# Optimization experiments

Hardware: AMD Instinct MI355X
Metric: run time of the kernel (lower is better)

The kernel has to match this reference:

```python
import jax, jax.numpy as jnp
import numpy as np

M, K, N = 8192, 4096, 4096

def setup_inputs() -> dict:
    key = jax.random.key(0)
    k0, k1, k2, k3, k4 = jax.random.split(key, 5)
    x = jax.random.normal(k0, (M, K), dtype=jnp.float32)
    # int8 weight stored as int32 spec dtype; values in [-127, 127]
    weight = jax.random.randint(k1, (N, K), -127, 128, dtype=jnp.int32)
    input_scale = jnp.array([0.02], dtype=jnp.float32)
    input_offset = jnp.zeros((1,), dtype=jnp.int32)
    # per-output-channel dequant scale (small positive)
    deq_scale = jax.random.uniform(k2, (N,), dtype=jnp.float32, minval=1e-4, maxval=2e-4)
    quant_bias = jax.random.randint(k3, (N,), -100, 101, dtype=jnp.int32)
    # sparse-compression output-channel reorder index (a permutation)
    index = jax.random.permutation(k4, N).astype(jnp.int32)
    return {"x": x, "weight": weight, "input_scale": input_scale,
            "input_offset": input_offset, "deq_scale": deq_scale,
            "quant_bias": quant_bias, "index": index}

def reference(x, weight, input_scale, input_offset, deq_scale, quant_bias, index):
    # 1) per-tensor activation quantization to int8
    x_q = jnp.clip(jnp.round(x / input_scale) + input_offset.astype(jnp.float32),
                   -128.0, 127.0).astype(jnp.int8)
    acc = jnp.matmul(x_q.astype(jnp.int32), weight.astype(jnp.int8).astype(jnp.int32).T)
    acc = acc + quant_bias  # [M, N] int32
    # 3) per-channel dequantization
    y = acc.astype(jnp.float32) * deq_scale  # [M, N]
    # 4) restore output-channel order from compressed layout
    return jnp.take(y, index, axis=-1)
```

## Files before the change

### kernel.cpp

```cpp
#include <hip/hip_runtime.h>
#include <hip/hip_bf16.h>
#include <stdint.h>

#define M_DIM 8192
#define K_DIM 4096
#define N_DIM 4096

#define BM 128
#define BN 128
#define BK 128

typedef int i32x4 __attribute__((ext_vector_type(4)));

__global__ __launch_bounds__(256) void quant_x_kernel(
    const float* __restrict__ x, const float* __restrict__ scale_p,
    const int* __restrict__ off_p, int8_t* __restrict__ xq)
{
    const float s = scale_p[0];
    const float off = (float)off_p[0];
    long base = ((long)blockIdx.x * 256 + threadIdx.x) * 16;
    const float4* xin = (const float4*)(x + base);
    float v[16];
    *(float4*)(v + 0)  = xin[0];
    *(float4*)(v + 4)  = xin[1];
    *(float4*)(v + 8)  = xin[2];
    *(float4*)(v + 12) = xin[3];
    uint32_t pk[4];
#pragma unroll
    for (int g = 0; g < 4; ++g) {
        uint32_t p = 0;
#pragma unroll
        for (int j = 0; j < 4; ++j) {
            float q = rintf(v[g * 4 + j] / s) + off;
            q = fminf(fmaxf(q, -128.0f), 127.0f);
            int qi = (int)q;
            p |= ((uint32_t)(qi & 0xff)) << (8 * j);
        }
        pk[g] = p;
    }
    uint4 o; o.x = pk[0]; o.y = pk[1]; o.z = pk[2]; o.w = pk[3];
    *(uint4*)(xq + base) = o;
}

__global__ __launch_bounds__(256) void pack_w_kernel(
    const int* __restrict__ w, const int* __restrict__ index,
    const float* __restrict__ deq, const int* __restrict__ qb,
    int8_t* __restrict__ bp, float* __restrict__ dsp, int* __restrict__ qbp)
{
    int j = blockIdx.x;
    int t = threadIdx.x;
    int src = index[j];
    const int4* wrow = (const int4*)(w + (long)src * K_DIM);
    uint32_t pk[4];
#pragma unroll
    for (int g = 0; g < 4; ++g) {
        int4 c = wrow[t * 4 + g];
        pk[g] = ((uint32_t)(c.x & 0xff)) | (((uint32_t)(c.y & 0xff)) << 8) |
                (((uint32_t)(c.z & 0xff)) << 16) | (((uint32_t)(c.w & 0xff)) << 24);
    }
    uint4 o; o.x = pk[0]; o.y = pk[1]; o.z = pk[2]; o.w = pk[3];
    *(uint4*)(bp + (long)j * K_DIM + t * 16) = o;
    if (t == 0) { dsp[j] = deq[src]; qbp[j] = qb[src]; }
}

__device__ __forceinline__ void gload_lds16(const void* g, void* l)
{
    __builtin_amdgcn_global_load_lds(
        (const __attribute__((address_space(1))) uint32_t*)g,
        (__attribute__((address_space(3))) uint32_t*)l, 16, 0, 0);
}

__global__ __launch_bounds__(256) void gemm_i8_kernel(
    const int8_t* __restrict__ A, const int8_t* __restrict__ B,
    const float* __restrict__ dsp, const int* __restrict__ qbp,
    float* __restrict__ C)
{
    __shared__ int8_t As[BM * BK];
    __shared__ int8_t Bs[BN * BK];

    int bid = blockIdx.x;
    int cpx = gridDim.x >> 3;
    int swz = (bid & 7) * cpx + (bid >> 3);
    int bn = swz % (N_DIM / BN);
    int bm = swz / (N_DIM / BN);
    int brow = bm * BM, bcol = bn * BN;

    int t = threadIdx.x;
    int l = t & 63;
    int wv = t >> 6;
    int wr = (wv >> 1) * 64;
    int wc = (wv & 1) * 64;

    const int8_t* ga[4];
    const int8_t* gb[4];
#pragma unroll
    for (int i = 0; i < 4; ++i) {
        int cid = i * 256 + t;
        int row = cid >> 3;
        int p = cid & 7;
        int lg = p ^ (row & 7);
        ga[i] = A + (long)(brow + row) * K_DIM + lg * 16;
        gb[i] = B + (long)(bcol + row) * K_DIM + lg * 16;
    }

    i32x4 acc[4][4] = {};

    for (int kt = 0; kt < K_DIM / BK; ++kt) {
#pragma unroll
        for (int i = 0; i < 4; ++i) {
            gload_lds16(ga[i], As + (i * 256 + t) * 16);
            ga[i] += BK;
        }
#pragma unroll
        for (int i = 0; i < 4; ++i) {
            gload_lds16(gb[i], Bs + (i * 256 + t) * 16);
            gb[i] += BK;
        }
        __syncthreads();

#pragma unroll
        for (int kk = 0; kk < 2; ++kk) {
            i32x4 af[4], bf[4];
#pragma unroll
            for (int m = 0; m < 4; ++m) {
                int row = wr + m * 16 + (l & 15);
                int slot = (kk * 4 + (l >> 4)) ^ (row & 7);
                af[m] = *(const i32x4*)(As + row * BK + slot * 16);
            }
#pragma unroll
            for (int n = 0; n < 4; ++n) {
                int row = wc + n * 16 + (l & 15);
                int slot = (kk * 4 + (l >> 4)) ^ (row & 7);
                bf[n] = *(const i32x4*)(Bs + row * BK + slot * 16);
            }
#pragma unroll
            for (int m = 0; m < 4; ++m)
#pragma unroll
                for (int n = 0; n < 4; ++n)
                    acc[m][n] = __builtin_amdgcn_mfma_i32_16x16x64_i8(
                        af[m], bf[n], acc[m][n], 0, 0, 0);
        }
        __syncthreads();
    }

#pragma unroll
    for (int n = 0; n < 4; ++n) {
        int gc = bcol + wc + n * 16 + (l & 15);
        float ds = dsp[gc];
        int qb = qbp[gc];
#pragma unroll
        for (int m = 0; m < 4; ++m) {
            int gr0 = brow + wr + m * 16 + ((l >> 4) * 4);
#pragma unroll
            for (int r = 0; r < 4; ++r) {
                float val = (float)(acc[m][n][r] + qb) * ds;
                C[(long)(gr0 + r) * N_DIM + gc] = val;
            }
        }
    }
}

extern "C" void kernel_launch(void* const* d_in, const int* in_sizes, int n_in,
                              void* d_out, int out_size, void* d_ws, size_t ws_size,
                              hipStream_t stream)
{
    (void)in_sizes; (void)n_in; (void)out_size; (void)ws_size;
    const float* x   = (const float*)d_in[0];
    const int*   w   = (const int*)d_in[1];
    const float* is  = (const float*)d_in[2];
    const int*   io  = (const int*)d_in[3];
    const float* dq  = (const float*)d_in[4];
    const int*   qb  = (const int*)d_in[5];
    const int*   idx = (const int*)d_in[6];
    float* out = (float*)d_out;

    int8_t* xq  = (int8_t*)d_ws;
    int8_t* bp  = xq + (size_t)M_DIM * K_DIM;
    float*  dsp = (float*)(bp + (size_t)N_DIM * K_DIM);
    int*    qbp = (int*)(dsp + N_DIM);

    long quant_blocks = ((long)M_DIM * K_DIM) / 16 / 256;
    quant_x_kernel<<<(int)quant_blocks, 256, 0, stream>>>(x, is, io, xq);
    pack_w_kernel<<<N_DIM, 256, 0, stream>>>(w, idx, dq, qb, bp, dsp, qbp);
    gemm_i8_kernel<<<(M_DIM / BM) * (N_DIM / BN), 256, 0, stream>>>(xq, bp, dsp, qbp, out);
}
```

Measured before the change: 209.9 us.

## Rework int8 GEMM into 256x256 tiles with triple-buffered LDS pipeline

The GEMM now uses 256x256 output tiles with BK=64, 512 threads (8 waves), and a three-stage LDS ring buffer. Global-to-LDS loads for stage kt+2 are interleaved with the MFMA work of stage kt, paced by explicit waitcnt, barriers, sched_barrier and setprio. The goal is to hide memory latency behind compute and raise arithmetic intensity per block. The cost is more LDS (96KB), more accumulator registers, and fewer blocks in the grid (512), which may hurt occupancy.

```diff
diff --git a/kernel.cpp b/kernel.cpp
--- a/kernel.cpp
+++ b/kernel.cpp
@@ -6,9 +6,12 @@
 #define K_DIM 4096
 #define N_DIM 4096
 
-#define BM 128
-#define BN 128
-#define BK 128
+#define BM 256
+#define BN 256
+#define BKB 64
+#define NT (K_DIM / BKB)
+#define ATILE (BM * BKB)
+#define BTILE (BN * BKB)
 
 typedef int i32x4 __attribute__((ext_vector_type(4)));
 
@@ -63,98 +66,133 @@
     if (t == 0) { dsp[j] = deq[src]; qbp[j] = qb[src]; }
 }
 
-__device__ __forceinline__ void gload_lds16(const void* g, void* l)
+__device__ __forceinline__ void gload_lds16(const int8_t* g, int8_t* l)
 {
     __builtin_amdgcn_global_load_lds(
         (const __attribute__((address_space(1))) uint32_t*)g,
         (__attribute__((address_space(3))) uint32_t*)l, 16, 0, 0);
 }
 
-__global__ __launch_bounds__(256) void gemm_i8_kernel(
+__global__ __launch_bounds__(512, 2) void gemm_i8_kernel(
     const int8_t* __restrict__ A, const int8_t* __restrict__ B,
     const float* __restrict__ dsp, const int* __restrict__ qbp,
     float* __restrict__ C)
 {
-    __shared__ int8_t As[BM * BK];
-    __shared__ int8_t Bs[BN * BK];
+    __shared__ int8_t lds[3][ATILE + BTILE];
 
     int bid = blockIdx.x;
-    int cpx = gridDim.x >> 3;
-    int swz = (bid & 7) * cpx + (bid >> 3);
-    int bn = swz % (N_DIM / BN);
-    int bm = swz / (N_DIM / BN);
+    int swz = (bid & 7) * (gridDim.x >> 3) + (bid >> 3);
+    int bm = swz & 31;
+    int bn = swz >> 5;
     int brow = bm * BM, bcol = bn * BN;
 
     int t = threadIdx.x;
-    int l = t & 63;
     int wv = t >> 6;
-    int wr = (wv >> 1) * 64;
-    int wc = (wv & 1) * 64;
-
-    const int8_t* ga[4];
-    const int8_t* gb[4];
-#pragma unroll
-    for (int i = 0; i < 4; ++i) {
-        int cid = i * 256 + t;
-        int row = cid >> 3;
-        int p = cid & 7;
-        int lg = p ^ (row & 7);
-        ga[i] = A + (long)(brow + row) * K_DIM + lg * 16;
-        gb[i] = B + (long)(bcol + row) * K_DIM + lg * 16;
-    }
-
-    i32x4 acc[4][4] = {};
-
-    for (int kt = 0; kt < K_DIM / BK; ++kt) {
-#pragma unroll
-        for (int i = 0; i < 4; ++i) {
-            gload_lds16(ga[i], As + (i * 256 + t) * 16);
-            ga[i] += BK;
-        }
-#pragma unroll
-        for (int i = 0; i < 4; ++i) {
-            gload_lds16(gb[i], Bs + (i * 256 + t) * 16);
-            gb[i] += BK;
-        }
-        __syncthreads();
-
-#pragma unroll
-        for (int kk = 0; kk < 2; ++kk) {
-            i32x4 af[4], bf[4];
-#pragma unroll
-            for (int m = 0; m < 4; ++m) {
-                int row = wr + m * 16 + (l & 15);
-                int slot = (kk * 4 + (l >> 4)) ^ (row & 7);
-                af[m] = *(const i32x4*)(As + row * BK + slot * 16);
-            }
-#pragma unroll
-            for (int n = 0; n < 4; ++n) {
-                int row = wc + n * 16 + (l & 15);
-                int slot = (kk * 4 + (l >> 4)) ^ (row & 7);
-                bf[n] = *(const i32x4*)(Bs + row * BK + slot * 16);
-            }
-#pragma unroll
-            for (int m = 0; m < 4; ++m)
-#pragma unroll
-                for (int n = 0; n < 4; ++n)
-                    acc[m][n] = __builtin_amdgcn_mfma_i32_16x16x64_i8(
-                        af[m], bf[n], acc[m][n], 0, 0, 0);
-        }
-        __syncthreads();
+    int l  = t & 63;
+    int lr = l & 15;
+    int ls = l >> 4;
+    int wrM = (wv >> 2) * 128;
+    int wcN = (wv & 3) * 64;
+    int pslot = ls ^ ((lr >> 1) & 3);
+
+    int aoff[8], boff[4];
+#pragma unroll
+    for (int m = 0; m < 8; ++m)
+        aoff[m] = (wrM + m * 16 + lr) * BKB + pslot * 16;
+#pragma unroll
+    for (int n = 0; n < 4; ++n)
+        boff[n] = ATILE + (wcN + n * 16 + lr) * BKB + pslot * 16;
+
+    const int8_t* sa[2]; int da[2];
+    const int8_t* sb[2]; int db[2];
+#pragma unroll
+    for (int i = 0; i < 2; ++i) {
+        int ca = i * 512 + t;
+        int row = ca >> 2;
+        int lg = (ca & 3) ^ ((row >> 1) & 3);
+        sa[i] = A + (long)(brow + row) * K_DIM + lg * 16;
+        da[i] = ca * 16;
+        sb[i] = B + (long)(bcol + row) * K_DIM + lg * 16;
+        db[i] = ATILE + ca * 16;
+    }
+
+#pragma unroll
+    for (int p = 0; p < 2; ++p) {
+        gload_lds16(sa[0], &lds[p][da[0]]);
+        gload_lds16(sa[1], &lds[p][da[1]]);
+        gload_lds16(sb[0], &lds[p][db[0]]);
+        gload_lds16(sb[1], &lds[p][db[1]]);
+        sa[0] += BKB; sa[1] += BKB; sb[0] += BKB; sb[1] += BKB;
+    }
+    asm volatile("s_waitcnt vmcnt(4)" ::: "memory");
+    __builtin_amdgcn_s_barrier();
+
+    i32x4 acc[8][4] = {};
+
+    for (int kt = 0; kt < NT; ++kt) {
+        const int cur = kt % 3;
+        const int stg = (kt + 2) % 3;
+        const bool do_stage = (kt + 2) < NT;
+        const int8_t* base = lds[cur];
+
+        i32x4 af[4], bf[4];
+
+#pragma unroll
+        for (int n = 0; n < 4; ++n) bf[n] = *(const i32x4*)(base + boff[n]);
+#pragma unroll
+        for (int m = 0; m < 4; ++m) af[m] = *(const i32x4*)(base + aoff[m]);
+        if (do_stage) {
+            gload_lds16(sa[0], &lds[stg][da[0]]);
+            gload_lds16(sa[1], &lds[stg][da[1]]);
+            sa[0] += BKB; sa[1] += BKB;
+        }
+        __builtin_amdgcn_s_barrier();
+        asm volatile("s_waitcnt lgkmcnt(0)" ::: "memory");
+        __builtin_amdgcn_sched_barrier(0);
+        __builtin_amdgcn_s_setprio(1);
+#pragma unroll
+        for (int m = 0; m < 4; ++m)
+#pragma unroll
+            for (int n = 0; n < 4; ++n)
+                acc[m][n] = __builtin_amdgcn_mfma_i32_16x16x64_i8(
+                    af[m], bf[n], acc[m][n], 0, 0, 0);
+        __builtin_amdgcn_s_setprio(0);
+        __builtin_amdgcn_s_barrier();
+
+#pragma unroll
+        for (int m = 0; m < 4; ++m) af[m] = *(const i32x4*)(base + aoff[m + 4]);
+        if (do_stage) {
+            gload_lds16(sb[0], &lds[stg][db[0]]);
+            gload_lds16(sb[1], &lds[stg][db[1]]);
+            sb[0] += BKB; sb[1] += BKB;
+        }
+        __builtin_amdgcn_s_barrier();
+        asm volatile("s_waitcnt lgkmcnt(0)" ::: "memory");
+        __builtin_amdgcn_sched_barrier(0);
+        __builtin_amdgcn_s_setprio(1);
+#pragma unroll
+        for (int m = 0; m < 4; ++m)
+#pragma unroll
+            for (int n = 0; n < 4; ++n)
+                acc[m + 4][n] = __builtin_amdgcn_mfma_i32_16x16x64_i8(
+                    af[m], bf[n], acc[m + 4][n], 0, 0, 0);
+        __builtin_amdgcn_s_setprio(0);
+        if (do_stage) asm volatile("s_waitcnt vmcnt(4)" ::: "memory");
+        else          asm volatile("s_waitcnt vmcnt(0)" ::: "memory");
+        __builtin_amdgcn_s_barrier();
     }
 
 #pragma unroll
     for (int n = 0; n < 4; ++n) {
-        int gc = bcol + wc + n * 16 + (l & 15);
+        int gc = bcol + wcN + n * 16 + lr;
         float ds = dsp[gc];
         int qb = qbp[gc];
 #pragma unroll
-        for (int m = 0; m < 4; ++m) {
-            int gr0 = brow + wr + m * 16 + ((l >> 4) * 4);
+        for (int m = 0; m < 8; ++m) {
+            int gr0 = brow + wrM + m * 16 + ls * 4;
 #pragma unroll
             for (int r = 0; r < 4; ++r) {
-                float val = (float)(acc[m][n][r] + qb) * ds;
-                C[(long)(gr0 + r) * N_DIM + gc] = val;
+                C[(long)(gr0 + r) * N_DIM + gc] = (float)(acc[m][n][r] + qb) * ds;
             }
         }
     }
@@ -182,5 +220,5 @@
     long quant_blocks = ((long)M_DIM * K_DIM) / 16 / 256;
     quant_x_kernel<<<(int)quant_blocks, 256, 0, stream>>>(x, is, io, xq);
     pack_w_kernel<<<N_DIM, 256, 0, stream>>>(w, idx, dq, qb, bp, dsp, qbp);
-    gemm_i8_kernel<<<(M_DIM / BM) * (N_DIM / BN), 256, 0, stream>>>(xq, bp, dsp, qbp, out);
-}
+    gemm_i8_kernel<<<(M_DIM / BM) * (N_DIM / BN), 512, 0, stream>>>(xq, bp, dsp, qbp, out);
+}
```

Result: faster. 201.6 us (-3.9%).
